# Kernel optimization log

Hardware: AMD Instinct MI355X
Metric: run time of the kernel (lower is better)

Reference implementation:

```python
import jax, jax.numpy as jnp
import numpy as np
import math

B, S, KV_DIM, Q_DIM, E, H = 16, 8192, 512, 512, 512, 8
D = E // H  # head_dim = 64


def setup_inputs() -> dict:
    key = jax.random.key(0)
    ks = jax.random.split(key, 12)
    s_q = 1.0 / math.sqrt(Q_DIM)
    s_kv = 1.0 / math.sqrt(KV_DIM)
    s_e = 1.0 / math.sqrt(E)
    return {
        "query": jax.random.normal(ks[0], (B, Q_DIM), dtype=jnp.float32),
        "key_value": jax.random.normal(ks[1], (B, S, KV_DIM), dtype=jnp.float32),
        "Wq": jax.random.uniform(ks[2], (Q_DIM, E), jnp.float32, -s_q, s_q),
        "bq": jax.random.uniform(ks[3], (E,), jnp.float32, -s_q, s_q),
        "Wk": jax.random.uniform(ks[4], (KV_DIM, E), jnp.float32, -s_kv, s_kv),
        "bk": jax.random.uniform(ks[5], (E,), jnp.float32, -s_kv, s_kv),
        "Wv": jax.random.uniform(ks[6], (KV_DIM, E), jnp.float32, -s_kv, s_kv),
        "bv": jax.random.uniform(ks[7], (E,), jnp.float32, -s_kv, s_kv),
        "Wo": jax.random.uniform(ks[8], (E, E), jnp.float32, -s_e, s_e),
        "bo": jax.random.uniform(ks[9], (E,), jnp.float32, -s_e, s_e),
    }


def reference(query, key_value, Wq, bq, Wk, bk, Wv, bv, Wo, bo):
    bsz, seq_len, _ = key_value.shape
    # q: [B, H, D] (single query per batch)
    q = (query @ Wq + bq).reshape(bsz, H, D)
    # k, v: [B, S, H, D]
    k = (key_value @ Wk + bk).reshape(bsz, seq_len, H, D)
    v = (key_value @ Wv + bv).reshape(bsz, seq_len, H, D)
    scale = 1.0 / math.sqrt(D)
    # attn logits: [B, H, S]
    attn = jnp.einsum("bhd,bshd->bhs", q, k) * scale
    weights = jax.nn.softmax(attn, axis=-1)
    # context: [B, H, D] -> [B, E]
    context = jnp.einsum("bhs,bshd->bhd", weights, v).reshape(bsz, E)
    return context @ Wo + bo
```

## Files before the change

kernel.cpp:

```cpp
#include <hip/hip_runtime.h>
#include <math.h>

#define B_   16
#define S_   8192
#define KVD  512
#define E_   512
#define H_   8
#define D_   64

#define OFF_QKVEC   0
#define OFF_LACC    65536
#define OFF_CTXACC  65664
#define OFF_CTXBUF  131200
#define ZERO_START  OFF_LACC
#define ZERO_COUNT  73856

__global__ __launch_bounds__(256) void k_prep(const float* __restrict__ query,
                                              const float* __restrict__ Wq,
                                              const float* __restrict__ bq,
                                              const float* __restrict__ Wk,
                                              float* __restrict__ wsf,
                                              float* __restrict__ out) {
    const int blk = blockIdx.x;
    const int tid = threadIdx.x;

    if (blk >= 64) {
        int i = (blk - 64) * 256 + tid;
        const int nws4 = ZERO_COUNT / 4;
        if (i < nws4) {
            *(float4*)&wsf[ZERO_START + i * 4] = make_float4(0.f, 0.f, 0.f, 0.f);
        } else if (i < nws4 + (B_ * E_) / 4) {
            *(float4*)&out[(size_t)(i - nws4) * 4] = make_float4(0.f, 0.f, 0.f, 0.f);
        }
        return;
    }

    const int cc = blk & 7, h = blk >> 3;
    float* qk_vec = wsf + OFF_QKVEC;

    __shared__ float qbuf[16 * 512];
    __shared__ float wk[64 * 65];
    __shared__ float qh[16 * 64];

    #pragma unroll
    for (int k = 0; k < 8; ++k) {
        int f4i = tid + k * 256;
        *(float4*)&qbuf[f4i * 4] = *(const float4*)&query[(size_t)f4i * 4];
    }
    #pragma unroll
    for (int k = 0; k < 4; ++k) {
        int f4i = tid + k * 256;
        int row = f4i >> 4, d4 = f4i & 15;
        float4 v = *(const float4*)&Wk[(size_t)(cc * 64 + row) * E_ + h * D_ + d4 * 4];
        wk[row * 65 + d4 * 4 + 0] = v.x;
        wk[row * 65 + d4 * 4 + 1] = v.y;
        wk[row * 65 + d4 * 4 + 2] = v.z;
        wk[row * 65 + d4 * 4 + 3] = v.w;
    }
    __syncthreads();

    const int d = tid & 63, w = tid >> 6;
    {
        float acc[4] = {0.f, 0.f, 0.f, 0.f};
        const float* wq = Wq + h * D_ + d;
        for (int k = 0; k < 512; k += 4) {
            #pragma unroll
            for (int kk = 0; kk < 4; ++kk) {
                float wv = wq[(size_t)(k + kk) * E_];
                #pragma unroll
                for (int i = 0; i < 4; ++i)
                    acc[i] = fmaf(qbuf[(w * 4 + i) * 512 + k + kk], wv, acc[i]);
            }
        }
        float bqv = bq[h * D_ + d];
        #pragma unroll
        for (int i = 0; i < 4; ++i)
            qh[(w * 4 + i) * 64 + d] = (acc[i] + bqv) * 0.125f;
    }
    __syncthreads();

    {
        const int c_local = tid & 63;
        float acc[4] = {0.f, 0.f, 0.f, 0.f};
        for (int dd = 0; dd < 64; ++dd) {
            float wv = wk[c_local * 65 + dd];
            #pragma unroll
            for (int i = 0; i < 4; ++i)
                acc[i] = fmaf(qh[(w * 4 + i) * 64 + dd], wv, acc[i]);
        }
        #pragma unroll
        for (int i = 0; i < 4; ++i) {
            int b = w * 4 + i;
            qk_vec[((size_t)b * H_ + h) * KVD + cc * 64 + c_local] = acc[i];
        }
    }
}

#define SROW 68
#define T_   8

__device__ __forceinline__ void stage_tile(const float* __restrict__ chunkbase,
                                           int t, float (&buf)[T_][KVD],
                                           int w, int lane) {
    #pragma unroll
    for (int r = 0; r < 2; ++r) {
        const int row = w * 2 + r;
        const float* rowp = chunkbase + (size_t)(t * T_ + row) * KVD;
        __builtin_amdgcn_global_load_lds(
            (__attribute__((address_space(1))) unsigned int*)(rowp + lane * 4),
            (__attribute__((address_space(3))) unsigned int*)(&buf[row][0]),
            16, 0, 0);
        __builtin_amdgcn_global_load_lds(
            (__attribute__((address_space(1))) unsigned int*)(rowp + 256 + lane * 4),
            (__attribute__((address_space(3))) unsigned int*)(&buf[row][256]),
            16, 0, 0);
    }
}

template <int NC>
__global__ __launch_bounds__(256, 2) void k_attn(const float* __restrict__ kv,
                                                 const float* __restrict__ qk_vec,
                                                 float* __restrict__ ctx_acc,
                                                 float* __restrict__ l_acc) {
    constexpr int CHUNK = S_ / NC;
    constexpr int NT = CHUNK / T_;

    __shared__ __align__(16) float kbuf[2][T_][KVD];
    __shared__ __align__(16) float scr[4][8][SROW];

    const int tid = threadIdx.x;
    const int lane = tid & 63;
    const int w = tid >> 6;
    const int nc = blockIdx.x, b = blockIdx.y;
    const int hme = lane >> 3, seg = lane & 7;
    const int g_mine = hme >> 1;
    (void)g_mine;

    float qk2[2][8];
    {
        const float* qb = qk_vec + ((size_t)b * H_ + 2 * w) * KVD;
        #pragma unroll
        for (int hh = 0; hh < 2; ++hh) {
            float4 v0 = *(const float4*)&qb[hh * KVD + lane * 4];
            float4 v1 = *(const float4*)&qb[hh * KVD + 256 + lane * 4];
            qk2[hh][0] = v0.x; qk2[hh][1] = v0.y; qk2[hh][2] = v0.z; qk2[hh][3] = v0.w;
            qk2[hh][4] = v1.x; qk2[hh][5] = v1.y; qk2[hh][6] = v1.z; qk2[hh][7] = v1.w;
        }
    }

    float ctx2[2][8];
    #pragma unroll
    for (int hh = 0; hh < 2; ++hh)
        #pragma unroll
        for (int j = 0; j < 8; ++j) ctx2[hh][j] = 0.f;
    float l_loc = 0.f;

    const float* chunkbase = kv + ((size_t)b * S_ + (size_t)nc * CHUNK) * KVD;

    stage_tile(chunkbase, 0, kbuf[0], w, lane);
    __syncthreads();

    int p = 0;
    #pragma unroll 1
    for (int t = 0; t < NT; ++t) {
        if (t + 1 < NT) stage_tile(chunkbase, t + 1, kbuf[p ^ 1], w, lane);
        #pragma unroll
        for (int g2 = 0; g2 < 2; ++g2) {
            const float(&rows)[T_][KVD] = kbuf[p];
            float kvr[4][8];
            #pragma unroll
            for (int r = 0; r < 4; ++r) {
                const float* rp = &rows[g2 * 4 + r][0];
                float4 v0 = *(const float4*)&rp[lane * 4];
                float4 v1 = *(const float4*)&rp[256 + lane * 4];
                kvr[r][0] = v0.x; kvr[r][1] = v0.y; kvr[r][2] = v0.z; kvr[r][3] = v0.w;
                kvr[r][4] = v1.x; kvr[r][5] = v1.y; kvr[r][6] = v1.z; kvr[r][7] = v1.w;
            }
            #pragma unroll
            for (int r = 0; r < 4; ++r)
                #pragma unroll
                for (int hh = 0; hh < 2; ++hh) {
                    float pp = 0.f;
                    #pragma unroll
                    for (int j = 0; j < 8; ++j)
                        pp = fmaf(kvr[r][j], qk2[hh][j], pp);
                    scr[w][r * 2 + hh][lane] = pp;
                }
            asm volatile("" ::: "memory");
            const float* gp = &scr[w][hme][seg * 8];
            float4 x = *(const float4*)gp;
            float4 y = *(const float4*)(gp + 4);
            float s = ((x.x + x.y) + (x.z + x.w)) + ((y.x + y.y) + (y.z + y.w));
            s += __shfl_xor(s, 1);
            s += __shfl_xor(s, 2);
            s += __shfl_xor(s, 4);
            float e = __expf(s);
            l_loc += e;
            #pragma unroll
            for (int r = 0; r < 4; ++r)
                #pragma unroll
                for (int hh = 0; hh < 2; ++hh) {
                    float wv = __shfl(e, (r * 2 + hh) * 8 + seg);
                    #pragma unroll
                    for (int j = 0; j < 8; ++j)
                        ctx2[hh][j] = fmaf(wv, kvr[r][j], ctx2[hh][j]);
                }
        }
        __syncthreads();
        p ^= 1;
    }

    {
        float ls = l_loc;
        ls += __shfl_xor(ls, 1);
        ls += __shfl_xor(ls, 2);
        ls += __shfl_xor(ls, 4);
        ls += __shfl_xor(ls, 16);
        ls += __shfl_xor(ls, 32);
        ls *= 0.125f;
        if (lane == 0) atomicAdd(&l_acc[b * H_ + 2 * w], ls);
        if (lane == 8) atomicAdd(&l_acc[b * H_ + 2 * w + 1], ls);
    }

    {
        size_t gb = (size_t)b * (H_ * KVD);
        #pragma unroll
        for (int hh = 0; hh < 2; ++hh) {
            float* dst = &ctx_acc[gb + (size_t)(2 * w + hh) * KVD];
            #pragma unroll
            for (int j = 0; j < 4; ++j)
                atomicAdd(&dst[lane * 4 + j], ctx2[hh][j]);
            #pragma unroll
            for (int j = 4; j < 8; ++j)
                atomicAdd(&dst[256 + lane * 4 + (j - 4)], ctx2[hh][j]);
        }
    }
}

__global__ __launch_bounds__(512) void k_ctx(const float* __restrict__ ctx_acc,
                                             const float* __restrict__ l_acc,
                                             const float* __restrict__ Wv,
                                             const float* __restrict__ bv,
                                             float* __restrict__ ctx_buf) {
    const int kc = blockIdx.x, b = blockIdx.y;
    const int e = threadIdx.x;
    const int h = e >> 6;
    const float inv = 1.0f / l_acc[b * H_ + h];
    const float* ca = ctx_acc + ((size_t)b * H_ + h) * KVD + kc * 128;
    const float* wv = Wv + (size_t)(kc * 128) * E_ + e;
    float a0 = 0.f, a1 = 0.f, a2 = 0.f, a3 = 0.f;
    for (int c = 0; c < 128; c += 4) {
        a0 = fmaf(ca[c],     wv[(size_t)(c)     * E_], a0);
        a1 = fmaf(ca[c + 1], wv[(size_t)(c + 1) * E_], a1);
        a2 = fmaf(ca[c + 2], wv[(size_t)(c + 2) * E_], a2);
        a3 = fmaf(ca[c + 3], wv[(size_t)(c + 3) * E_], a3);
    }
    float val = ((a0 + a1) + (a2 + a3)) * inv;
    if (kc == 0) val += bv[e];
    atomicAdd(&ctx_buf[(size_t)b * E_ + e], val);
}

__global__ __launch_bounds__(512) void k_o(const float* __restrict__ ctx_buf,
                                           const float* __restrict__ Wo,
                                           const float* __restrict__ bo,
                                           float* __restrict__ out) {
    const int kc = blockIdx.x, b = blockIdx.y;
    const int e = threadIdx.x;
    const float* cs = ctx_buf + (size_t)b * E_ + kc * 128;
    const float* wo = Wo + (size_t)(kc * 128) * E_ + e;
    float a0 = 0.f, a1 = 0.f, a2 = 0.f, a3 = 0.f;
    for (int k = 0; k < 128; k += 4) {
        a0 = fmaf(cs[k],     wo[(size_t)(k)     * E_], a0);
        a1 = fmaf(cs[k + 1], wo[(size_t)(k + 1) * E_], a1);
        a2 = fmaf(cs[k + 2], wo[(size_t)(k + 2) * E_], a2);
        a3 = fmaf(cs[k + 3], wo[(size_t)(k + 3) * E_], a3);
    }
    float val = (a0 + a1) + (a2 + a3);
    if (kc == 0) val += bo[e];
    atomicAdd(&out[(size_t)b * E_ + e], val);
}

extern "C" void kernel_launch(void* const* d_in, const int* in_sizes, int n_in,
                              void* d_out, int out_size, void* d_ws, size_t ws_size,
                              hipStream_t stream) {
    const float* query = (const float*)d_in[0];
    const float* kv    = (const float*)d_in[1];
    const float* Wq    = (const float*)d_in[2];
    const float* bq    = (const float*)d_in[3];
    const float* Wk    = (const float*)d_in[4];
    const float* Wv    = (const float*)d_in[6];
    const float* bv    = (const float*)d_in[7];
    const float* Wo    = (const float*)d_in[8];
    const float* bo    = (const float*)d_in[9];
    float* out = (float*)d_out;
    float* wsf = (float*)d_ws;

    float* qk_vec  = wsf + OFF_QKVEC;
    float* l_acc   = wsf + OFF_LACC;
    float* ctx_acc = wsf + OFF_CTXACC;
    float* ctx_buf = wsf + OFF_CTXBUF;

    constexpr int NC = 32;

    k_prep<<<145, 256, 0, stream>>>(query, Wq, bq, Wk, wsf, out);
    k_attn<NC><<<dim3(NC, B_), 256, 0, stream>>>(kv, qk_vec, ctx_acc, l_acc);
    k_ctx<<<dim3(4, B_), 512, 0, stream>>>(ctx_acc, l_acc, Wv, bv, ctx_buf);
    k_o<<<dim3(4, B_), 512, 0, stream>>>(ctx_buf, Wo, bo, out);
}
```

Baseline: 432.4 us.

## Use 8 waves per attention block with one head per wave

The attention kernel goes from 256 to 512 threads per block. Each of the 8 wavefronts now owns one head instead of two and processes the whole 8-row tile at once. Each wave stages one row into LDS, so per-thread register state for query and context drops by half. The costs are that every wave reads all 8 LDS rows per tile, which doubles the LDS read traffic per row, and that block-wide barriers now span more waves.

Measured after the change: 437.6 us. About the same (+1.2%).

```diff
diff --git a/kernel.cpp b/kernel.cpp
--- a/kernel.cpp
+++ b/kernel.cpp
@@ -99,26 +99,22 @@
 #define SROW 68
 #define T_   8
 
-__device__ __forceinline__ void stage_tile(const float* __restrict__ chunkbase,
-                                           int t, float (&buf)[T_][KVD],
-                                           int w, int lane) {
-    #pragma unroll
-    for (int r = 0; r < 2; ++r) {
-        const int row = w * 2 + r;
-        const float* rowp = chunkbase + (size_t)(t * T_ + row) * KVD;
-        __builtin_amdgcn_global_load_lds(
-            (__attribute__((address_space(1))) unsigned int*)(rowp + lane * 4),
-            (__attribute__((address_space(3))) unsigned int*)(&buf[row][0]),
-            16, 0, 0);
-        __builtin_amdgcn_global_load_lds(
-            (__attribute__((address_space(1))) unsigned int*)(rowp + 256 + lane * 4),
-            (__attribute__((address_space(3))) unsigned int*)(&buf[row][256]),
-            16, 0, 0);
-    }
+__device__ __forceinline__ void stage_tile8(const float* __restrict__ chunkbase,
+                                            int t, float (&buf)[T_][KVD],
+                                            int w, int lane) {
+    const float* rowp = chunkbase + (size_t)(t * T_ + w) * KVD;
+    __builtin_amdgcn_global_load_lds(
+        (__attribute__((address_space(1))) unsigned int*)(rowp + lane * 4),
+        (__attribute__((address_space(3))) unsigned int*)(&buf[w][0]),
+        16, 0, 0);
+    __builtin_amdgcn_global_load_lds(
+        (__attribute__((address_space(1))) unsigned int*)(rowp + 256 + lane * 4),
+        (__attribute__((address_space(3))) unsigned int*)(&buf[w][256]),
+        16, 0, 0);
 }
 
 template <int NC>
-__global__ __launch_bounds__(256, 2) void k_attn(const float* __restrict__ kv,
+__global__ __launch_bounds__(512, 4) void k_attn(const float* __restrict__ kv,
                                                  const float* __restrict__ qk_vec,
                                                  float* __restrict__ ctx_acc,
                                                  float* __restrict__ l_acc) {
@@ -126,85 +122,70 @@
     constexpr int NT = CHUNK / T_;
 
     __shared__ __align__(16) float kbuf[2][T_][KVD];
-    __shared__ __align__(16) float scr[4][8][SROW];
+    __shared__ __align__(16) float scr[8][T_][SROW];
 
     const int tid = threadIdx.x;
     const int lane = tid & 63;
     const int w = tid >> 6;
     const int nc = blockIdx.x, b = blockIdx.y;
     const int hme = lane >> 3, seg = lane & 7;
-    const int g_mine = hme >> 1;
-    (void)g_mine;
-
-    float qk2[2][8];
-    {
-        const float* qb = qk_vec + ((size_t)b * H_ + 2 * w) * KVD;
-        #pragma unroll
-        for (int hh = 0; hh < 2; ++hh) {
-            float4 v0 = *(const float4*)&qb[hh * KVD + lane * 4];
-            float4 v1 = *(const float4*)&qb[hh * KVD + 256 + lane * 4];
-            qk2[hh][0] = v0.x; qk2[hh][1] = v0.y; qk2[hh][2] = v0.z; qk2[hh][3] = v0.w;
-            qk2[hh][4] = v1.x; qk2[hh][5] = v1.y; qk2[hh][6] = v1.z; qk2[hh][7] = v1.w;
-        }
-    }
-
-    float ctx2[2][8];
+
+    float qk1[8];
+    {
+        const float* qb = qk_vec + ((size_t)b * H_ + w) * KVD;
+        float4 v0 = *(const float4*)&qb[lane * 4];
+        float4 v1 = *(const float4*)&qb[256 + lane * 4];
+        qk1[0] = v0.x; qk1[1] = v0.y; qk1[2] = v0.z; qk1[3] = v0.w;
+        qk1[4] = v1.x; qk1[5] = v1.y; qk1[6] = v1.z; qk1[7] = v1.w;
+    }
+
+    float ctx1[8];
     #pragma unroll
-    for (int hh = 0; hh < 2; ++hh)
-        #pragma unroll
-        for (int j = 0; j < 8; ++j) ctx2[hh][j] = 0.f;
+    for (int j = 0; j < 8; ++j) ctx1[j] = 0.f;
     float l_loc = 0.f;
 
     const float* chunkbase = kv + ((size_t)b * S_ + (size_t)nc * CHUNK) * KVD;
 
-    stage_tile(chunkbase, 0, kbuf[0], w, lane);
+    stage_tile8(chunkbase, 0, kbuf[0], w, lane);
     __syncthreads();
 
     int p = 0;
     #pragma unroll 1
     for (int t = 0; t < NT; ++t) {
-        if (t + 1 < NT) stage_tile(chunkbase, t + 1, kbuf[p ^ 1], w, lane);
-        #pragma unroll
-        for (int g2 = 0; g2 < 2; ++g2) {
-            const float(&rows)[T_][KVD] = kbuf[p];
-            float kvr[4][8];
-            #pragma unroll
-            for (int r = 0; r < 4; ++r) {
-                const float* rp = &rows[g2 * 4 + r][0];
-                float4 v0 = *(const float4*)&rp[lane * 4];
-                float4 v1 = *(const float4*)&rp[256 + lane * 4];
-                kvr[r][0] = v0.x; kvr[r][1] = v0.y; kvr[r][2] = v0.z; kvr[r][3] = v0.w;
-                kvr[r][4] = v1.x; kvr[r][5] = v1.y; kvr[r][6] = v1.z; kvr[r][7] = v1.w;
-            }
-            #pragma unroll
-            for (int r = 0; r < 4; ++r)
-                #pragma unroll
-                for (int hh = 0; hh < 2; ++hh) {
-                    float pp = 0.f;
-                    #pragma unroll
-                    for (int j = 0; j < 8; ++j)
-                        pp = fmaf(kvr[r][j], qk2[hh][j], pp);
-                    scr[w][r * 2 + hh][lane] = pp;
-                }
-            asm volatile("" ::: "memory");
-            const float* gp = &scr[w][hme][seg * 8];
-            float4 x = *(const float4*)gp;
-            float4 y = *(const float4*)(gp + 4);
-            float s = ((x.x + x.y) + (x.z + x.w)) + ((y.x + y.y) + (y.z + y.w));
-            s += __shfl_xor(s, 1);
-            s += __shfl_xor(s, 2);
-            s += __shfl_xor(s, 4);
-            float e = __expf(s);
-            l_loc += e;
-            #pragma unroll
-            for (int r = 0; r < 4; ++r)
-                #pragma unroll
-                for (int hh = 0; hh < 2; ++hh) {
-                    float wv = __shfl(e, (r * 2 + hh) * 8 + seg);
-                    #pragma unroll
-                    for (int j = 0; j < 8; ++j)
-                        ctx2[hh][j] = fmaf(wv, kvr[r][j], ctx2[hh][j]);
-                }
+        if (t + 1 < NT) stage_tile8(chunkbase, t + 1, kbuf[p ^ 1], w, lane);
+
+        float kvr[T_][8];
+        #pragma unroll
+        for (int r = 0; r < T_; ++r) {
+            const float* rp = &kbuf[p][r][0];
+            float4 v0 = *(const float4*)&rp[lane * 4];
+            float4 v1 = *(const float4*)&rp[256 + lane * 4];
+            kvr[r][0] = v0.x; kvr[r][1] = v0.y; kvr[r][2] = v0.z; kvr[r][3] = v0.w;
+            kvr[r][4] = v1.x; kvr[r][5] = v1.y; kvr[r][6] = v1.z; kvr[r][7] = v1.w;
+        }
+        #pragma unroll
+        for (int r = 0; r < T_; ++r) {
+            float pp = 0.f;
+            #pragma unroll
+            for (int j = 0; j < 8; ++j) pp = fmaf(kvr[r][j], qk1[j], pp);
+            scr[w][r][lane] = pp;
+        }
+        asm volatile("" ::: "memory");
+        const float* gp = &scr[w][hme][seg * 8];
+        float4 x = *(const float4*)gp;
+        float4 y = *(const float4*)(gp + 4);
+        float s = ((x.x + x.y) + (x.z + x.w)) + ((y.x + y.y) + (y.z + y.w));
+        s += __shfl_xor(s, 1);
+        s += __shfl_xor(s, 2);
+        s += __shfl_xor(s, 4);
+        float e = __expf(s);
+        l_loc += e;
+        #pragma unroll
+        for (int r = 0; r < T_; ++r) {
+            float wv = __shfl(e, r * 8 + seg);
+            #pragma unroll
+            for (int j = 0; j < 8; ++j)
+                ctx1[j] = fmaf(wv, kvr[r][j], ctx1[j]);
         }
         __syncthreads();
         p ^= 1;
@@ -215,25 +196,21 @@
         ls += __shfl_xor(ls, 1);
         ls += __shfl_xor(ls, 2);
         ls += __shfl_xor(ls, 4);
+        ls += __shfl_xor(ls, 8);
         ls += __shfl_xor(ls, 16);
         ls += __shfl_xor(ls, 32);
         ls *= 0.125f;
-        if (lane == 0) atomicAdd(&l_acc[b * H_ + 2 * w], ls);
-        if (lane == 8) atomicAdd(&l_acc[b * H_ + 2 * w + 1], ls);
-    }
-
-    {
-        size_t gb = (size_t)b * (H_ * KVD);
-        #pragma unroll
-        for (int hh = 0; hh < 2; ++hh) {
-            float* dst = &ctx_acc[gb + (size_t)(2 * w + hh) * KVD];
-            #pragma unroll
-            for (int j = 0; j < 4; ++j)
-                atomicAdd(&dst[lane * 4 + j], ctx2[hh][j]);
-            #pragma unroll
-            for (int j = 4; j < 8; ++j)
-                atomicAdd(&dst[256 + lane * 4 + (j - 4)], ctx2[hh][j]);
-        }
+        if (lane == 0) atomicAdd(&l_acc[b * H_ + w], ls);
+    }
+
+    {
+        float* dst = &ctx_acc[(size_t)(b * H_ + w) * KVD];
+        #pragma unroll
+        for (int j = 0; j < 4; ++j)
+            atomicAdd(&dst[lane * 4 + j], ctx1[j]);
+        #pragma unroll
+        for (int j = 4; j < 8; ++j)
+            atomicAdd(&dst[256 + lane * 4 + (j - 4)], ctx1[j]);
     }
 }
 
@@ -303,7 +280,7 @@
     constexpr int NC = 32;
 
     k_prep<<<145, 256, 0, stream>>>(query, Wq, bq, Wk, wsf, out);
-    k_attn<NC><<<dim3(NC, B_), 256, 0, stream>>>(kv, qk_vec, ctx_acc, l_acc);
+    k_attn<NC><<<dim3(NC, B_), 512, 0, stream>>>(kv, qk_vec, ctx_acc, l_acc);
     k_ctx<<<dim3(4, B_), 512, 0, stream>>>(ctx_acc, l_acc, Wv, bv, ctx_buf);
     k_o<<<dim3(4, B_), 512, 0, stream>>>(ctx_buf, Wo, bo, out);
 }
```
